# Kernel tuning notes

Hardware: AMD Instinct MI355X
Metric: run time of the kernel (lower is better)

## Reference

```python
import jax, jax.numpy as jnp
import numpy as np


def setup_inputs() -> dict:
    key = jax.random.key(0)
    N, C, E, S = 200000, 128, 3200000, 5000
    k0, k1, k2 = jax.random.split(key, 3)
    x = jax.random.normal(k0, (N, C), dtype=jnp.float32)
    edge_index = jax.random.randint(k1, (2, E), 0, N, dtype=jnp.int32)
    starts = (jnp.arange(S, dtype=jnp.int32) * (N // S))  # sorted sentence start offsets
    node1_indices = starts
    node2_indices = starts + 1
    sent_indices = starts + 2
    W = jax.random.normal(k2, (C, 1), dtype=jnp.float32) * 0.1
    b = jnp.zeros((1,), dtype=jnp.float32)
    return dict(x=x, edge_index=edge_index, node1_indices=node1_indices,
                node2_indices=node2_indices, sent_indices=sent_indices,
                W=W, b=b, alpha=4)


def _gcn_score(x, edge_index, W, b):
    # PyG GCNConv: h = xW; add self-loops; sym-normalized aggregation; + bias
    N = x.shape[0]
    h = x @ W  # [N, 1]
    row, col = edge_index[0], edge_index[1]
    ones = jnp.ones(row.shape[0], dtype=x.dtype)
    deg = jax.ops.segment_sum(ones, col, num_segments=N) + 1.0  # self-loop included
    dis = jax.lax.rsqrt(deg)
    norm = dis[row] * dis[col]
    agg = jax.ops.segment_sum(h[row] * norm[:, None], col, num_segments=N)
    out = agg + h * (dis * dis)[:, None]  # self-loop term, norm = 1/deg
    return (out + b).squeeze(-1)  # [N]


def reference(x, edge_index, node1_indices, node2_indices, sent_indices, W, b, alpha):
    N = x.shape[0]
    S = node1_indices.shape[0]
    score = _gcn_score(x, edge_index, W, b)  # [N]

    # per-sentence segment ids: segment i = [node1_indices[i], node1_indices[i+1])
    seg = jnp.searchsorted(node1_indices, jnp.arange(N, dtype=node1_indices.dtype), side='right') - 1
    seg = jnp.clip(seg, 0, S - 1)

    # numerically-stable per-segment softmax of scores
    m = jax.ops.segment_max(score, seg, num_segments=S)
    e = jnp.exp(score - m[seg])
    Z = jax.ops.segment_sum(e, seg, num_segments=S)
    p = e / Z[seg]  # normalized scores per sentence

    # cutoff = max(p) - alpha * std(p) per sentence (population std, as np.std)
    cnt = jax.ops.segment_sum(jnp.ones(N, dtype=p.dtype), seg, num_segments=S)
    pmax = jax.ops.segment_max(p, seg, num_segments=S)
    mean = jax.ops.segment_sum(p, seg, num_segments=S) / cnt
    var = jax.ops.segment_sum(p * p, seg, num_segments=S) / cnt - mean * mean
    std = jnp.sqrt(jnp.maximum(var, 0.0))
    cutoff = pmax - jnp.float32(alpha) * std
    keep = p >= cutoff[seg]

    # union with node1/node2/sent special nodes (always kept)
    keep = keep.at[node1_indices].set(True)
    keep = keep.at[node2_indices].set(True)
    keep = keep.at[sent_indices].set(True)

    # remap: position of each kept node in the compacted ordering
    pos = jnp.cumsum(keep.astype(jnp.int32)) - 1  # valid only where keep

    # gated node features (masked-dense form of x[perm] * tanh(score[perm]))
    x_out = jnp.where(keep[:, None], x * jnp.tanh(score)[:, None], 0.0)

    new_node1 = pos[node1_indices]
    new_node2 = pos[node2_indices]
    new_sent = pos[sent_indices]

    # filter_adj: keep edges with both endpoints kept, remap endpoints
    row, col = edge_index[0], edge_index[1]
    edge_keep = keep[row] & keep[col]
    new_edge_index = jnp.where(edge_keep[None, :], pos[edge_index], -1)

    return (x_out, new_edge_index, keep, edge_keep, new_node1, new_node2, new_sent)
```

## Files before the change

### kernel.cpp

```cpp
#include <hip/hip_runtime.h>
#include <math.h>

#define FXSCALE 4398046511104.0
#define WINDOW 1984
#define NBMAX 128
#define BINB 2048
#define SCAN_CHUNK 2048

typedef float vfloat4 __attribute__((ext_vector_type(4)));

__global__ void k_hist(const int* __restrict__ ecol, int* __restrict__ binCnt,
                       int E, int NB) {
    __shared__ int cnt[NBMAX];
    int tid = threadIdx.x;
    for (int i = tid; i < NBMAX; i += 256) cnt[i] = 0;
    __syncthreads();
    for (long e = (long)blockIdx.x * 256 + tid; e < E; e += 512L * 256)
        atomicAdd(&cnt[ecol[e] / WINDOW], 1);
    __syncthreads();
    for (int i = tid; i < NB; i += 256)
        if (cnt[i] > 0) atomicAdd(&binCnt[i], cnt[i]);
}

__global__ void k_bin_h(const int* __restrict__ erow, const int* __restrict__ ecol,
                        const int* __restrict__ binCnt, int* __restrict__ binWr0,
                        int* __restrict__ binnedRow,
                        unsigned short* __restrict__ binnedCol16,
                        const float* __restrict__ x, const float* __restrict__ W,
                        double* __restrict__ h,
                        int E, int NB, int N, int C, int nBatches) {
    int blk = blockIdx.x;
    if (blk >= nBatches) {
        int t = (blk - nBatches) * 256 + threadIdx.x;
        int row = t >> 5;
        int lane = t & 31;
        if (row >= N) return;
        const float4* xr = (const float4*)(x + (size_t)row * C);
        const float4* w4 = (const float4*)W;
        int C4 = C >> 2;
        double acc = 0.0;
        for (int c = lane; c < C4; c += 32) {
            float4 xv = xr[c];
            float4 wv = w4[c];
            acc += (double)xv.x * (double)wv.x + (double)xv.y * (double)wv.y
                 + (double)xv.z * (double)wv.z + (double)xv.w * (double)wv.w;
        }
        #pragma unroll
        for (int o = 16; o > 0; o >>= 1) acc += __shfl_xor(acc, o);
        if (lane == 0) h[row] = acc;
        return;
    }
    __shared__ int cnt[NBMAX];
    __shared__ int lbase[NBMAX];
    __shared__ int gbase[NBMAX];
    __shared__ int lrow[BINB];
    __shared__ unsigned short lcol[BINB];
    __shared__ unsigned char lbin[BINB];
    int tid = threadIdx.x;
    for (int i = tid; i < NBMAX; i += 256) cnt[i] = 0;
    __syncthreads();
    long b0 = (long)blk * BINB;
    int n = (int)((E - b0) < (long)BINB ? (E - b0) : (long)BINB);
    int bA[8], rkA[8], rwA[8];
    unsigned short clA[8];
    #pragma unroll
    for (int k = 0; k < 8; k++) bA[k] = -1;
    int base_i = tid * 8;
    if (base_i + 8 <= n) {
        long e = b0 + base_i;
        int4 r0 = *(const int4*)(erow + e), r1 = *(const int4*)(erow + e + 4);
        int4 c0 = *(const int4*)(ecol + e), c1 = *(const int4*)(ecol + e + 4);
        int rr[8] = {r0.x, r0.y, r0.z, r0.w, r1.x, r1.y, r1.z, r1.w};
        int cc[8] = {c0.x, c0.y, c0.z, c0.w, c1.x, c1.y, c1.z, c1.w};
        #pragma unroll
        for (int k = 0; k < 8; k++) {
            int c = cc[k];
            int bb = c / WINDOW;
            bA[k] = bb; rwA[k] = rr[k]; clA[k] = (unsigned short)(c - bb * WINDOW);
            rkA[k] = atomicAdd(&cnt[bb], 1);
        }
    } else {
        for (int k = 0; k < 8; k++) {
            int i = base_i + k;
            if (i < n) {
                long e = b0 + i;
                int c = ecol[e];
                int bb = c / WINDOW;
                bA[k] = bb; rwA[k] = erow[e]; clA[k] = (unsigned short)(c - bb * WINDOW);
                rkA[k] = atomicAdd(&cnt[bb], 1);
            }
        }
    }
    __syncthreads();
    if (tid == 0) {
        int acc = 0;
        #pragma unroll 1
        for (int i = 0; i < NB; i++) { lbase[i] = acc; acc += cnt[i]; }
    }
    __syncthreads();
    if (tid < NB && cnt[tid] > 0) {
        int boff = 0;
        for (int i = 0; i < tid; i++) boff += binCnt[i];
        gbase[tid] = boff + atomicAdd(&binWr0[tid], cnt[tid]);
    }
    __syncthreads();
    #pragma unroll
    for (int k = 0; k < 8; k++) {
        if (bA[k] >= 0) {
            int l = lbase[bA[k]] + rkA[k];
            lrow[l] = rwA[k];
            lcol[l] = clA[k];
            lbin[l] = (unsigned char)bA[k];
        }
    }
    __syncthreads();
    for (int l = tid; l < n; l += 256) {
        int bb = lbin[l];
        int g = gbase[bb] + (l - lbase[bb]);
        binnedRow[g] = lrow[l];
        binnedCol16[g] = lcol[l];
    }
}

__global__ void k_degb(const unsigned short* __restrict__ binnedCol16,
                       const int* __restrict__ binCnt,
                       unsigned int* __restrict__ partialDeg, int N, int Md, int NB) {
    __shared__ unsigned int cnt[WINDOW];
    __shared__ int boff[2];
    int bin = blockIdx.x / Md, m = blockIdx.x % Md;
    int tid = threadIdx.x;
    if (tid == 0) {
        int acc = 0;
        for (int i = 0; i < bin; i++) acc += binCnt[i];
        boff[0] = acc;
        boff[1] = acc + binCnt[bin];
    }
    for (int i = tid; i < WINDOW; i += 256) cnt[i] = 0;
    __syncthreads();
    int st = boff[0], en = boff[1];
    for (int idx = st + m * 256 + tid; idx < en; idx += Md * 256)
        atomicAdd(&cnt[binnedCol16[idx]], 1u);
    __syncthreads();
    int wb = bin * WINDOW;
    int wlim = (N - wb) < WINDOW ? (N - wb) : WINDOW;
    for (int i = tid; i < wlim; i += 256)
        partialDeg[(size_t)m * N + wb + i] = cnt[i];
}

__global__ void k_dis_hd(const unsigned int* __restrict__ partialDeg,
                         const double* __restrict__ h,
                         double* __restrict__ dis, double* __restrict__ hd,
                         int N, int Md) {
    int i = blockIdx.x * blockDim.x + threadIdx.x;
    if (i >= N) return;
    unsigned int dsum = 0;
    for (int m = 0; m < Md; m++) dsum += partialDeg[(size_t)m * N + i];
    double d = 1.0 / sqrt((double)dsum + 1.0);
    dis[i] = d;
    hd[i] = h[i] * d;
}

__global__ void k_aggb(const int* __restrict__ binnedRow,
                       const unsigned short* __restrict__ binnedCol16,
                       const int* __restrict__ binCnt,
                       const double* __restrict__ hd, const double* __restrict__ dis,
                       unsigned long long* __restrict__ partialAgg, int N, int Ma, int NB) {
    __shared__ unsigned long long acc[WINDOW];
    __shared__ int boff[2];
    int bin = blockIdx.x / Ma, m = blockIdx.x % Ma;
    int tid = threadIdx.x;
    if (tid == 0) {
        int a = 0;
        for (int i = 0; i < bin; i++) a += binCnt[i];
        boff[0] = a;
        boff[1] = a + binCnt[bin];
    }
    for (int i = tid; i < WINDOW; i += 256) acc[i] = 0ULL;
    __syncthreads();
    int st = boff[0], en = boff[1];
    int wb = bin * WINDOW;
    for (int idx = st + m * 256 + tid; idx < en; idx += Ma * 256) {
        int r = binnedRow[idx];
        int c16 = binnedCol16[idx];
        long long q = __double2ll_rn(hd[r] * dis[wb + c16] * FXSCALE);
        atomicAdd(&acc[c16], (unsigned long long)q);
    }
    __syncthreads();
    int wlim = (N - wb) < WINDOW ? (N - wb) : WINDOW;
    for (int i = tid; i < wlim; i += 256)
        partialAgg[(size_t)m * N + wb + i] = acc[i];
}

__global__ void k_score(const unsigned long long* __restrict__ partialAgg,
                        const double* __restrict__ h, const double* __restrict__ dis,
                        const float* __restrict__ bptr,
                        float* __restrict__ score32, float* __restrict__ tg,
                        int N, int Ma) {
    int i = blockIdx.x * blockDim.x + threadIdx.x;
    if (i >= N) return;
    long long acc = 0;
    for (int m = 0; m < Ma; m++) acc += (long long)partialAgg[(size_t)m * N + i];
    double agg = (double)acc / FXSCALE;
    double d = dis[i];
    double sc = (agg + h[i] * (d * d)) + (double)bptr[0];
    score32[i] = (float)sc;
    tg[i] = (float)tanh(sc);
}

__global__ void k_seg_np(const float* __restrict__ score32, const int* __restrict__ starts,
                         float* __restrict__ p32, int* __restrict__ keepI,
                         const int* __restrict__ alphaPtr,
                         const int* __restrict__ n1, const int* __restrict__ n2,
                         const int* __restrict__ sent, int N, int S) {
    int g = blockIdx.x * blockDim.x + threadIdx.x;
    if (g >= S) return;
    int st = starts[g];
    int en = (g == S - 1) ? N : starts[g + 1];
    if (en <= st) return;

    int ai = alphaPtr[0];
    float alpha = (ai >= 0 && ai < 1000000) ? (float)ai : __int_as_float(ai);

    float m = -3.402823466e38f;
    for (int i = st; i < en; i++) m = fmaxf(m, score32[i]);

    float Z = 0.0f;
    for (int i = st; i < en; i++) {
        float dm = __fsub_rn(score32[i], m);
        float e = (float)exp((double)dm);
        p32[i] = e;
        Z = __fadd_rn(Z, e);
    }

    float sp = 0.0f, sq = 0.0f, pm = -3.402823466e38f;
    for (int i = st; i < en; i++) {
        float p = __fdiv_rn(p32[i], Z);
        p32[i] = p;
        sp = __fadd_rn(sp, p);
        sq = __fadd_rn(sq, __fmul_rn(p, p));
        pm = fmaxf(pm, p);
    }

    float cnt_ = (float)(en - st);
    float mean = __fdiv_rn(sp, cnt_);
    float var = __fsub_rn(__fdiv_rn(sq, cnt_), __fmul_rn(mean, mean));
    float sd = sqrtf(fmaxf(var, 0.0f));
    float cutoff = __fsub_rn(pm, __fmul_rn(alpha, sd));

    for (int i = st; i < en; i++) keepI[i] = (p32[i] >= cutoff) ? 1 : 0;

    keepI[n1[g]] = 1;
    keepI[n2[g]] = 1;
    keepI[sent[g]] = 1;
}

__global__ void k_scan(const int* __restrict__ keepI, const float* __restrict__ tg,
                       unsigned long long* __restrict__ stArr,
                       float* __restrict__ posF, float* __restrict__ gate,
                       float* __restrict__ o_keep, int N) {
    int tid = threadIdx.x;
    int b = blockIdx.x;
    long base = (long)b * SCAN_CHUNK + (long)tid * 8;
    int v[8];
    int th = 0;
    #pragma unroll
    for (int k = 0; k < 8; k++) {
        long i = base + k;
        v[k] = (i < N) ? keepI[i] : 0;
        th += v[k];
    }
    __shared__ int sm[256];
    sm[tid] = th; __syncthreads();
    for (int off = 1; off < 256; off <<= 1) {
        int t = (tid >= off) ? sm[tid - off] : 0;
        __syncthreads();
        sm[tid] += t;
        __syncthreads();
    }
    int total = sm[255];
    __shared__ int exclSh;
    if (tid == 0) {
        if (b == 0) {
            atomicExch(&stArr[0], (2ULL << 62) | (unsigned long long)(unsigned)total);
            exclSh = 0;
        } else {
            atomicExch(&stArr[b], (1ULL << 62) | (unsigned long long)(unsigned)total);
            int excl = 0;
            int j = b - 1;
            while (true) {
                unsigned long long s = atomicAdd(&stArr[j], 0ULL);
                unsigned state = (unsigned)(s >> 62);
                if (state == 0) continue;
                excl += (int)(s & 0x3FFFFFFFFFFFFFFFULL);
                if (state == 2u) break;
                j--;
            }
            atomicExch(&stArr[b], (2ULL << 62) | (unsigned long long)(unsigned)(excl + total));
            exclSh = excl;
        }
    }
    __syncthreads();
    int run = exclSh + sm[tid] - th;
    #pragma unroll
    for (int k = 0; k < 8; k++) {
        long i = base + k;
        if (i < N) {
            posF[i] = v[k] ? (float)(run + v[k] - 1) : -1.0f;
            gate[i] = v[k] ? tg[i] : 0.0f;
            o_keep[i] = v[k] ? 1.0f : 0.0f;
            run += v[k];
        }
    }
}

__global__ void k_out(const float4* __restrict__ x4, const float* __restrict__ gate,
                      float* __restrict__ o_x, long total4,
                      const int* __restrict__ erow, const int* __restrict__ ecol,
                      const float* __restrict__ posF,
                      float* __restrict__ o_edge, float* __restrict__ o_ekeep, int E,
                      const int* __restrict__ n1, const int* __restrict__ n2,
                      const int* __restrict__ sent,
                      float* __restrict__ o_n1, float* __restrict__ o_n2,
                      float* __restrict__ o_sent, int S,
                      int nxb, int neb4) {
    int b = blockIdx.x;
    if (b < nxb) {
        long idx = (long)b * blockDim.x + threadIdx.x;
        if (idx >= total4) return;
        int row = (int)(idx >> 5);
        float g = gate[row];
        float4 v = x4[idx];
        vfloat4 r = { v.x * g, v.y * g, v.z * g, v.w * g };
        __builtin_nontemporal_store(r, (vfloat4*)o_x + idx);
    } else if (b < nxb + neb4) {
        long e0 = ((long)(b - nxb) * blockDim.x + threadIdx.x) * 4;
        if (e0 >= E) return;
        if (e0 + 3 < E) {
            int4 r4 = *(const int4*)(erow + e0);
            int4 c4 = *(const int4*)(ecol + e0);
            vfloat4 oer, oec, ok;
            #pragma unroll
            for (int k = 0; k < 4; k++) {
                int r = (&r4.x)[k], c = (&c4.x)[k];
                float pr = posF[r], pc = posF[c];
                bool ek = (pr >= 0.0f) && (pc >= 0.0f);
                oer[k] = ek ? pr : -1.0f;
                oec[k] = ek ? pc : -1.0f;
                ok[k]  = ek ? 1.0f : 0.0f;
            }
            __builtin_nontemporal_store(oer, (vfloat4*)(o_edge + e0));
            __builtin_nontemporal_store(oec, (vfloat4*)(o_edge + (size_t)E + e0));
            __builtin_nontemporal_store(ok,  (vfloat4*)(o_ekeep + e0));
        } else {
            for (long e = e0; e < E; e++) {
                int r = erow[e], c = ecol[e];
                float pr = posF[r], pc = posF[c];
                bool ek = (pr >= 0.0f) && (pc >= 0.0f);
                o_edge[e] = ek ? pr : -1.0f;
                o_edge[(size_t)E + e] = ek ? pc : -1.0f;
                o_ekeep[e] = ek ? 1.0f : 0.0f;
            }
        }
    } else {
        int i = (b - nxb - neb4) * blockDim.x + threadIdx.x;
        if (i >= S) return;
        o_n1[i] = posF[n1[i]];
        o_n2[i] = posF[n2[i]];
        o_sent[i] = posF[sent[i]];
    }
}

extern "C" void kernel_launch(void* const* d_in, const int* in_sizes, int n_in,
                              void* d_out, int out_size, void* d_ws, size_t ws_size,
                              hipStream_t stream) {
    const float* x    = (const float*)d_in[0];
    const int*   eidx = (const int*)d_in[1];
    const int*   n1   = (const int*)d_in[2];
    const int*   n2   = (const int*)d_in[3];
    const int*   sent = (const int*)d_in[4];
    const float* W    = (const float*)d_in[5];
    const float* bp   = (const float*)d_in[6];
    const int*   alphaPtr = (const int*)d_in[7];

    int C = in_sizes[5];
    int N = in_sizes[0] / C;
    int E = in_sizes[1] / 2;
    int S = in_sizes[2];

    const int* erow = eidx;
    const int* ecol = eidx + E;

    int NB = (N + WINDOW - 1) / WINDOW;
    const int Md = 8, Ma = 8;

    char* ws = (char*)d_ws;
    size_t off = 0;
    auto alloc = [&](size_t bytes) { void* p = ws + off; off += (bytes + 255) & ~(size_t)255; return p; };
    int*   binCnt = (int*)  alloc(NBMAX * 4);
    int*   binWr0 = (int*)  alloc(NBMAX * 4);
    unsigned long long* scanSt = (unsigned long long*)alloc(256 * 8);
    size_t zeroBytes = (size_t)((char*)(scanSt + 256) - (char*)binCnt);
    int*   binnedRow = (int*)alloc((size_t)E * 4);
    unsigned short* binnedCol16 = (unsigned short*)alloc((size_t)E * 2);
    unsigned int* partialDeg = (unsigned int*)alloc((size_t)Md * N * 4);
    unsigned long long* partialAgg = (unsigned long long*)alloc((size_t)Ma * N * 8);
    double* h     = (double*)alloc((size_t)N * 8);
    double* dis   = (double*)alloc((size_t)N * 8);
    double* hd    = (double*)alloc((size_t)N * 8);
    float* score32 = (float*)alloc((size_t)N * 4);
    float* p32    = (float*)alloc((size_t)N * 4);
    float* tg     = (float*)alloc((size_t)N * 4);
    int*   keepI  = (int*)  alloc((size_t)N * 4);
    float* posF   = (float*)alloc((size_t)N * 4);
    float* gate   = (float*)alloc((size_t)N * 4);

    float* o_x     = (float*)d_out;
    float* o_edge  = o_x + (size_t)N * C;
    float* o_keep  = o_edge + 2 * (size_t)E;
    float* o_ekeep = o_keep + N;
    float* o_n1    = o_ekeep + E;
    float* o_n2    = o_n1 + S;
    float* o_sent  = o_n2 + S;

    (void)hipMemsetAsync(binCnt, 0, zeroBytes, stream);

    k_hist<<<512, 256, 0, stream>>>(ecol, binCnt, E, NB);
    int nBatches = (int)(((long)E + BINB - 1) / BINB);
    int nhb = (N * 32 + 255) / 256;
    k_bin_h<<<nBatches + nhb, 256, 0, stream>>>(erow, ecol, binCnt, binWr0,
                                                binnedRow, binnedCol16,
                                                x, W, h, E, NB, N, C, nBatches);
    k_degb<<<NB * Md, 256, 0, stream>>>(binnedCol16, binCnt, partialDeg, N, Md, NB);
    k_dis_hd<<<(N + 255) / 256, 256, 0, stream>>>(partialDeg, h, dis, hd, N, Md);
    k_aggb<<<NB * Ma, 256, 0, stream>>>(binnedRow, binnedCol16, binCnt, hd, dis, partialAgg, N, Ma, NB);
    k_score<<<(N + 255) / 256, 256, 0, stream>>>(partialAgg, h, dis, bp, score32, tg, N, Ma);
    k_seg_np<<<(S + 255) / 256, 256, 0, stream>>>(score32, n1, p32, keepI, alphaPtr, n1, n2, sent, N, S);
    int nb = (N + SCAN_CHUNK - 1) / SCAN_CHUNK;
    k_scan<<<nb, 256, 0, stream>>>(keepI, tg, scanSt, posF, gate, o_keep, N);

    long total4 = (long)N * (C / 4);
    int nxb = (int)((total4 + 255) / 256);
    long e4 = (E + 3) / 4;
    int neb4 = (int)((e4 + 255) / 256);
    int nsb = (S + 255) / 256;
    k_out<<<nxb + neb4 + nsb, 256, 0, stream>>>(
        (const float4*)x, gate, o_x, total4,
        erow, ecol, posF, o_edge, o_ekeep, E,
        n1, n2, sent, o_n1, o_n2, o_sent, S, nxb, neb4);
}
```

Before: 251.7 us.

## Fuse segment softmax and keep-scan into one LDS-staged kernel; cache bin counts in LDS

Merges the per-sentence softmax/cutoff kernel and the compaction scan kernel into a single kernel. Each block handles 256 sentences, stages their scores in LDS, computes keep flags and per-segment kept counts, then runs a block scan plus a decoupled lookback to write positions, gates and keep outputs. This removes one launch and the global round trips of the intermediate p and keep arrays. Separately, the bin-count prefix sums in the binning, degree and aggregation kernels now read from an LDS copy of binCnt instead of looping over global memory. The cost is that each segment is still processed serially by one thread, and only 20 blocks run, so there is little parallelism.

```diff
diff --git a/kernel.cpp b/kernel.cpp
--- a/kernel.cpp
+++ b/kernel.cpp
@@ -5,7 +5,7 @@
 #define WINDOW 1984
 #define NBMAX 128
 #define BINB 2048
-#define SCAN_CHUNK 2048
+#define LDSCAP 12288
 
 typedef float vfloat4 __attribute__((ext_vector_type(4)));
 
@@ -51,13 +51,14 @@
         return;
     }
     __shared__ int cnt[NBMAX];
+    __shared__ int bcS[NBMAX];
     __shared__ int lbase[NBMAX];
     __shared__ int gbase[NBMAX];
     __shared__ int lrow[BINB];
     __shared__ unsigned short lcol[BINB];
     __shared__ unsigned char lbin[BINB];
     int tid = threadIdx.x;
-    for (int i = tid; i < NBMAX; i += 256) cnt[i] = 0;
+    for (int i = tid; i < NBMAX; i += 256) { cnt[i] = 0; bcS[i] = (i < NB) ? binCnt[i] : 0; }
     __syncthreads();
     long b0 = (long)blk * BINB;
     int n = (int)((E - b0) < (long)BINB ? (E - b0) : (long)BINB);
@@ -100,7 +101,7 @@
     __syncthreads();
     if (tid < NB && cnt[tid] > 0) {
         int boff = 0;
-        for (int i = 0; i < tid; i++) boff += binCnt[i];
+        for (int i = 0; i < tid; i++) boff += bcS[i];
         gbase[tid] = boff + atomicAdd(&binWr0[tid], cnt[tid]);
     }
     __syncthreads();
@@ -126,16 +127,19 @@
                        const int* __restrict__ binCnt,
                        unsigned int* __restrict__ partialDeg, int N, int Md, int NB) {
     __shared__ unsigned int cnt[WINDOW];
+    __shared__ int bcS[NBMAX];
     __shared__ int boff[2];
     int bin = blockIdx.x / Md, m = blockIdx.x % Md;
     int tid = threadIdx.x;
+    for (int i = tid; i < NB; i += 256) bcS[i] = binCnt[i];
+    for (int i = tid; i < WINDOW; i += 256) cnt[i] = 0;
+    __syncthreads();
     if (tid == 0) {
         int acc = 0;
-        for (int i = 0; i < bin; i++) acc += binCnt[i];
+        for (int i = 0; i < bin; i++) acc += bcS[i];
         boff[0] = acc;
-        boff[1] = acc + binCnt[bin];
-    }
-    for (int i = tid; i < WINDOW; i += 256) cnt[i] = 0;
+        boff[1] = acc + bcS[bin];
+    }
     __syncthreads();
     int st = boff[0], en = boff[1];
     for (int idx = st + m * 256 + tid; idx < en; idx += Md * 256)
@@ -166,16 +170,19 @@
                        const double* __restrict__ hd, const double* __restrict__ dis,
                        unsigned long long* __restrict__ partialAgg, int N, int Ma, int NB) {
     __shared__ unsigned long long acc[WINDOW];
+    __shared__ int bcS[NBMAX];
     __shared__ int boff[2];
     int bin = blockIdx.x / Ma, m = blockIdx.x % Ma;
     int tid = threadIdx.x;
+    for (int i = tid; i < NB; i += 256) bcS[i] = binCnt[i];
+    for (int i = tid; i < WINDOW; i += 256) acc[i] = 0ULL;
+    __syncthreads();
     if (tid == 0) {
         int a = 0;
-        for (int i = 0; i < bin; i++) a += binCnt[i];
+        for (int i = 0; i < bin; i++) a += bcS[i];
         boff[0] = a;
-        boff[1] = a + binCnt[bin];
-    }
-    for (int i = tid; i < WINDOW; i += 256) acc[i] = 0ULL;
+        boff[1] = a + bcS[bin];
+    }
     __syncthreads();
     int st = boff[0], en = boff[1];
     int wb = bin * WINDOW;
@@ -207,78 +214,121 @@
     tg[i] = (float)tanh(sc);
 }
 
-__global__ void k_seg_np(const float* __restrict__ score32, const int* __restrict__ starts,
-                         float* __restrict__ p32, int* __restrict__ keepI,
-                         const int* __restrict__ alphaPtr,
-                         const int* __restrict__ n1, const int* __restrict__ n2,
-                         const int* __restrict__ sent, int N, int S) {
-    int g = blockIdx.x * blockDim.x + threadIdx.x;
-    if (g >= S) return;
-    int st = starts[g];
-    int en = (g == S - 1) ? N : starts[g + 1];
-    if (en <= st) return;
+__global__ void k_seg_scan(const float* __restrict__ score32, const float* __restrict__ tg,
+                           const int* __restrict__ starts, const int* __restrict__ alphaPtr,
+                           const int* __restrict__ n1, const int* __restrict__ n2,
+                           const int* __restrict__ sent,
+                           unsigned long long* __restrict__ stArr,
+                           float* __restrict__ p32, int* __restrict__ keepG,
+                           float* __restrict__ posF, float* __restrict__ gate,
+                           float* __restrict__ o_keep, int N, int S) {
+    __shared__ float scoreS[LDSCAP];
+    __shared__ float pS[LDSCAP];
+    __shared__ int smc[256];
+    __shared__ int exclSh;
+    int tid = threadIdx.x;
+    int b = blockIdx.x;
+    int g0 = b * 256;
+    int segs = S - g0; if (segs > 256) segs = 256;
+    int st0 = starts[g0];
+    int en0 = (g0 + 256 >= S) ? N : starts[g0 + 256];
+    int len = en0 - st0;
+    bool useLds = (len <= LDSCAP);
 
     int ai = alphaPtr[0];
     float alpha = (ai >= 0 && ai < 1000000) ? (float)ai : __int_as_float(ai);
 
-    float m = -3.402823466e38f;
-    for (int i = st; i < en; i++) m = fmaxf(m, score32[i]);
-
-    float Z = 0.0f;
-    for (int i = st; i < en; i++) {
-        float dm = __fsub_rn(score32[i], m);
-        float e = (float)exp((double)dm);
-        p32[i] = e;
-        Z = __fadd_rn(Z, e);
-    }
-
-    float sp = 0.0f, sq = 0.0f, pm = -3.402823466e38f;
-    for (int i = st; i < en; i++) {
-        float p = __fdiv_rn(p32[i], Z);
-        p32[i] = p;
-        sp = __fadd_rn(sp, p);
-        sq = __fadd_rn(sq, __fmul_rn(p, p));
-        pm = fmaxf(pm, p);
-    }
-
-    float cnt_ = (float)(en - st);
-    float mean = __fdiv_rn(sp, cnt_);
-    float var = __fsub_rn(__fdiv_rn(sq, cnt_), __fmul_rn(mean, mean));
-    float sd = sqrtf(fmaxf(var, 0.0f));
-    float cutoff = __fsub_rn(pm, __fmul_rn(alpha, sd));
-
-    for (int i = st; i < en; i++) keepI[i] = (p32[i] >= cutoff) ? 1 : 0;
-
-    keepI[n1[g]] = 1;
-    keepI[n2[g]] = 1;
-    keepI[sent[g]] = 1;
-}
-
-__global__ void k_scan(const int* __restrict__ keepI, const float* __restrict__ tg,
-                       unsigned long long* __restrict__ stArr,
-                       float* __restrict__ posF, float* __restrict__ gate,
-                       float* __restrict__ o_keep, int N) {
-    int tid = threadIdx.x;
-    int b = blockIdx.x;
-    long base = (long)b * SCAN_CHUNK + (long)tid * 8;
-    int v[8];
-    int th = 0;
-    #pragma unroll
-    for (int k = 0; k < 8; k++) {
-        long i = base + k;
-        v[k] = (i < N) ? keepI[i] : 0;
-        th += v[k];
-    }
-    __shared__ int sm[256];
-    sm[tid] = th; __syncthreads();
-    for (int off = 1; off < 256; off <<= 1) {
-        int t = (tid >= off) ? sm[tid - off] : 0;
+    int myKept = 0;
+    int myStL = 0, myEnL = 0;
+    bool active = false;
+
+    if (useLds) {
+        for (int i = tid; i < len; i += 256) scoreS[i] = score32[st0 + i];
         __syncthreads();
-        sm[tid] += t;
+        int g = g0 + tid;
+        if (tid < segs) {
+            int st = starts[g] - st0;
+            int en = ((g == S - 1) ? N : starts[g + 1]) - st0;
+            if (en > st) {
+                active = true; myStL = st; myEnL = en;
+                float m = -3.402823466e38f;
+                for (int i = st; i < en; i++) m = fmaxf(m, scoreS[i]);
+                float Z = 0.0f;
+                for (int i = st; i < en; i++) {
+                    float dm = __fsub_rn(scoreS[i], m);
+                    float e = (float)exp((double)dm);
+                    pS[i] = e;
+                    Z = __fadd_rn(Z, e);
+                }
+                float sp = 0.0f, sq = 0.0f, pm = -3.402823466e38f;
+                for (int i = st; i < en; i++) {
+                    float p = __fdiv_rn(pS[i], Z);
+                    pS[i] = p;
+                    sp = __fadd_rn(sp, p);
+                    sq = __fadd_rn(sq, __fmul_rn(p, p));
+                    pm = fmaxf(pm, p);
+                }
+                float cnt_ = (float)(en - st);
+                float mean = __fdiv_rn(sp, cnt_);
+                float var = __fsub_rn(__fdiv_rn(sq, cnt_), __fmul_rn(mean, mean));
+                float sd = sqrtf(fmaxf(var, 0.0f));
+                float cutoff = __fsub_rn(pm, __fmul_rn(alpha, sd));
+                for (int i = st; i < en; i++)
+                    scoreS[i] = (pS[i] >= cutoff) ? 1.0f : 0.0f;
+                scoreS[n1[g] - st0] = 1.0f;
+                scoreS[n2[g] - st0] = 1.0f;
+                scoreS[sent[g] - st0] = 1.0f;
+                int c = 0;
+                for (int i = st; i < en; i++) c += (scoreS[i] != 0.0f) ? 1 : 0;
+                myKept = c;
+            }
+        }
+    } else {
+        int g = g0 + tid;
+        if (tid < segs) {
+            int st = starts[g];
+            int en = (g == S - 1) ? N : starts[g + 1];
+            if (en > st) {
+                active = true; myStL = st - st0; myEnL = en - st0;
+                float m = -3.402823466e38f;
+                for (int i = st; i < en; i++) m = fmaxf(m, score32[i]);
+                float Z = 0.0f;
+                for (int i = st; i < en; i++) {
+                    float dm = __fsub_rn(score32[i], m);
+                    float e = (float)exp((double)dm);
+                    p32[i] = e;
+                    Z = __fadd_rn(Z, e);
+                }
+                float sp = 0.0f, sq = 0.0f, pm = -3.402823466e38f;
+                for (int i = st; i < en; i++) {
+                    float p = __fdiv_rn(p32[i], Z);
+                    p32[i] = p;
+                    sp = __fadd_rn(sp, p);
+                    sq = __fadd_rn(sq, __fmul_rn(p, p));
+                    pm = fmaxf(pm, p);
+                }
+                float cnt_ = (float)(en - st);
+                float mean = __fdiv_rn(sp, cnt_);
+                float var = __fsub_rn(__fdiv_rn(sq, cnt_), __fmul_rn(mean, mean));
+                float sd = sqrtf(fmaxf(var, 0.0f));
+                float cutoff = __fsub_rn(pm, __fmul_rn(alpha, sd));
+                for (int i = st; i < en; i++) keepG[i] = (p32[i] >= cutoff) ? 1 : 0;
+                keepG[n1[g]] = 1; keepG[n2[g]] = 1; keepG[sent[g]] = 1;
+                int c = 0;
+                for (int i = st; i < en; i++) c += keepG[i];
+                myKept = c;
+            }
+        }
+    }
+    smc[tid] = myKept;
+    __syncthreads();
+    for (int off2 = 1; off2 < 256; off2 <<= 1) {
+        int t = (tid >= off2) ? smc[tid - off2] : 0;
         __syncthreads();
-    }
-    int total = sm[255];
-    __shared__ int exclSh;
+        smc[tid] += t;
+        __syncthreads();
+    }
+    int total = smc[255];
     if (tid == 0) {
         if (b == 0) {
             atomicExch(&stArr[0], (2ULL << 62) | (unsigned long long)(unsigned)total);
@@ -300,16 +350,27 @@
         }
     }
     __syncthreads();
-    int run = exclSh + sm[tid] - th;
-    #pragma unroll
-    for (int k = 0; k < 8; k++) {
-        long i = base + k;
-        if (i < N) {
-            posF[i] = v[k] ? (float)(run + v[k] - 1) : -1.0f;
-            gate[i] = v[k] ? tg[i] : 0.0f;
-            o_keep[i] = v[k] ? 1.0f : 0.0f;
-            run += v[k];
-        }
+    if (active) {
+        int run = exclSh + smc[tid] - myKept;
+        if (useLds) {
+            for (int i = myStL; i < myEnL; i++) {
+                if (scoreS[i] != 0.0f) { pS[i] = (float)run; run++; }
+                else pS[i] = -1.0f;
+            }
+        } else {
+            for (int i = myStL; i < myEnL; i++) {
+                if (keepG[st0 + i]) { p32[st0 + i] = (float)run; run++; }
+                else p32[st0 + i] = -1.0f;
+            }
+        }
+    }
+    __syncthreads();
+    for (int i = tid; i < len; i += 256) {
+        float pv = useLds ? pS[i] : p32[st0 + i];
+        bool v = (pv >= 0.0f);
+        posF[st0 + i] = pv;
+        o_keep[st0 + i] = v ? 1.0f : 0.0f;
+        gate[st0 + i] = v ? tg[st0 + i] : 0.0f;
     }
 }
 
@@ -392,14 +453,16 @@
 
     int NB = (N + WINDOW - 1) / WINDOW;
     const int Md = 8, Ma = 8;
+    int nsegb = (S + 255) / 256;
+    int stN = nsegb > 256 ? nsegb : 256;
 
     char* ws = (char*)d_ws;
     size_t off = 0;
     auto alloc = [&](size_t bytes) { void* p = ws + off; off += (bytes + 255) & ~(size_t)255; return p; };
     int*   binCnt = (int*)  alloc(NBMAX * 4);
     int*   binWr0 = (int*)  alloc(NBMAX * 4);
-    unsigned long long* scanSt = (unsigned long long*)alloc(256 * 8);
-    size_t zeroBytes = (size_t)((char*)(scanSt + 256) - (char*)binCnt);
+    unsigned long long* scanSt = (unsigned long long*)alloc((size_t)stN * 8);
+    size_t zeroBytes = (size_t)((char*)(scanSt + stN) - (char*)binCnt);
     int*   binnedRow = (int*)alloc((size_t)E * 4);
     unsigned short* binnedCol16 = (unsigned short*)alloc((size_t)E * 2);
     unsigned int* partialDeg = (unsigned int*)alloc((size_t)Md * N * 4);
@@ -410,7 +473,7 @@
     float* score32 = (float*)alloc((size_t)N * 4);
     float* p32    = (float*)alloc((size_t)N * 4);
     float* tg     = (float*)alloc((size_t)N * 4);
-    int*   keepI  = (int*)  alloc((size_t)N * 4);
+    int*   keepG  = (int*)  alloc((size_t)N * 4);
     float* posF   = (float*)alloc((size_t)N * 4);
     float* gate   = (float*)alloc((size_t)N * 4);
 
@@ -434,9 +497,8 @@
     k_dis_hd<<<(N + 255) / 256, 256, 0, stream>>>(partialDeg, h, dis, hd, N, Md);
     k_aggb<<<NB * Ma, 256, 0, stream>>>(binnedRow, binnedCol16, binCnt, hd, dis, partialAgg, N, Ma, NB);
     k_score<<<(N + 255) / 256, 256, 0, stream>>>(partialAgg, h, dis, bp, score32, tg, N, Ma);
-    k_seg_np<<<(S + 255) / 256, 256, 0, stream>>>(score32, n1, p32, keepI, alphaPtr, n1, n2, sent, N, S);
-    int nb = (N + SCAN_CHUNK - 1) / SCAN_CHUNK;
-    k_scan<<<nb, 256, 0, stream>>>(keepI, tg, scanSt, posF, gate, o_keep, N);
+    k_seg_scan<<<nsegb, 256, 0, stream>>>(score32, tg, n1, alphaPtr, n1, n2, sent,
+                                          scanSt, p32, keepG, posF, gate, o_keep, N, S);
 
     long total4 = (long)N * (C / 4);
     int nxb = (int)((total4 + 255) / 256);
```

Result: faster. 232.9 us (-7.5%).
